# Optimization experiments

Hardware: AMD Instinct MI355X
Metric: run time of the kernel (lower is better)

Reference implementation:

```python
import jax, jax.numpy as jnp
import numpy as np

B, T, C, H = 16, 512, 1080, 20  # batch, seq, embd, heads; head_dim = C // H = 54

def setup_inputs() -> dict:
    key = jax.random.key(0)
    k1, k2, k3, k4, k5 = jax.random.split(key, 5)
    s = 0.02
    return {
        "x": jax.random.normal(k1, (B, T, C), dtype=jnp.float32),
        "W_attn": jax.random.normal(k2, (C, 3 * C), dtype=jnp.float32) * s,
        "b_attn": jax.random.normal(k3, (3 * C,), dtype=jnp.float32) * s,
        "W_proj": jax.random.normal(k4, (C, C), dtype=jnp.float32) * s,
        "b_proj": jax.random.normal(k5, (C,), dtype=jnp.float32) * s,
    }

def reference(x, W_attn, b_attn, W_proj, b_proj):
    Bb, Tt, Cc = x.shape
    hd = Cc // H
    qkv = jnp.einsum('btc,cd->btd', x, W_attn) + b_attn  # [B,T,3C]
    q, k, v = jnp.split(qkv, 3, axis=2)
    # [B,T,C] -> [B,H,T,hd]
    q = q.reshape(Bb, Tt, H, hd).transpose(0, 2, 1, 3)
    k = k.reshape(Bb, Tt, H, hd).transpose(0, 2, 1, 3)
    v = v.reshape(Bb, Tt, H, hd).transpose(0, 2, 1, 3)
    att = jnp.einsum('bhqd,bhkd->bhqk', q, k) * (1.0 / jnp.sqrt(jnp.float32(hd)))
    causal = jnp.tril(jnp.ones((Tt, Tt), dtype=bool))
    att = jnp.where(causal, att, -jnp.inf)
    att = jax.nn.softmax(att, axis=-1)
    y = jnp.einsum('bhqk,bhkd->bhqd', att, v)  # [B,H,T,hd]
    y = y.transpose(0, 2, 1, 3).reshape(Bb, Tt, Cc)
    return jnp.einsum('btc,cd->btd', y, W_proj) + b_proj
```

## Files before the change

kernel.cpp:

```cpp
#include <hip/hip_runtime.h>
#include <hip/hip_bf16.h>

#define B_   16
#define T_   512
#define C_   1080
#define H_   20
#define HD_  54
#define DP_  64
#define M_   (B_ * T_)
#define KP_  1088
#define NT_  17
#define NQKV_ 3840
#define NPRJ_ 1152
#define NBT_ (B_ * H_ * T_)

typedef short bf16x8 __attribute__((ext_vector_type(8)));
typedef float f32x4  __attribute__((ext_vector_type(4)));
typedef unsigned short u16x8 __attribute__((ext_vector_type(8)));

__device__ __forceinline__ void gload_lds16(const void* g, void* l) {
    __builtin_amdgcn_global_load_lds(
        (const __attribute__((address_space(1))) void*)g,
        (__attribute__((address_space(3))) void*)l,
        16, 0, 0);
}

__device__ __forceinline__ unsigned short f2b(float x) {
    return __builtin_bit_cast(unsigned short, __float2bfloat16(x));
}

__global__ __launch_bounds__(256) void cvt_pad(
    const float* __restrict__ src, __hip_bfloat16* __restrict__ dst)
{
    int idx = blockIdx.x * 256 + threadIdx.x;
    if (idx >= M_ * (KP_ / 4)) return;
    int m = idx / (KP_ / 4), c = idx - m * (KP_ / 4);
    ushort4 o;
    if (c < C_ / 4) {
        float4 v = *reinterpret_cast<const float4*>(src + (size_t)m * C_ + c * 4);
        o.x = f2b(v.x); o.y = f2b(v.y); o.z = f2b(v.z); o.w = f2b(v.w);
    } else {
        o.x = o.y = o.z = o.w = 0;
    }
    *reinterpret_cast<ushort4*>(reinterpret_cast<unsigned short*>(dst) + (size_t)m * KP_ + c * 4) = o;
}

__global__ __launch_bounds__(256) void transpose_wqkv(
    const float* __restrict__ W, __hip_bfloat16* __restrict__ Wt)
{
    __shared__ float tile[32][33];
    int n0 = blockIdx.x * 32, k0 = blockIdx.y * 32;
    int tx = threadIdx.x, ty = threadIdx.y;
    int np = n0 + tx;
    int which = np / 1280;
    int rem = np - which * 1280;
    int h = rem >> 6, d = rem & 63;
    int sn = which * C_ + h * HD_ + d;
    bool valid = d < HD_;
    #pragma unroll
    for (int i = 0; i < 32; i += 8) {
        int k = k0 + ty + i;
        tile[ty + i][tx] = (valid && k < C_) ? W[(size_t)k * (3 * C_) + sn] : 0.f;
    }
    __syncthreads();
    #pragma unroll
    for (int i = 0; i < 32; i += 8) {
        int n = n0 + ty + i, k = k0 + tx;
        Wt[(size_t)n * KP_ + k] = __float2bfloat16(tile[tx][ty + i]);
    }
}

__global__ __launch_bounds__(256) void transpose_w(
    const float* __restrict__ W, __hip_bfloat16* __restrict__ Wt,
    int K, int N, int Kp)
{
    __shared__ float tile[32][33];
    int n0 = blockIdx.x * 32, k0 = blockIdx.y * 32;
    int tx = threadIdx.x, ty = threadIdx.y;
    #pragma unroll
    for (int i = 0; i < 32; i += 8) {
        int k = k0 + ty + i, n = n0 + tx;
        tile[ty + i][tx] = (k < K && n < N) ? W[(size_t)k * N + n] : 0.f;
    }
    __syncthreads();
    #pragma unroll
    for (int i = 0; i < 32; i += 8) {
        int n = n0 + ty + i, k = k0 + tx;
        Wt[(size_t)n * Kp + k] = __float2bfloat16(tile[tx][ty + i]);
    }
}

__global__ __launch_bounds__(256) void build_bias(
    const float* __restrict__ b_attn, float* __restrict__ bp)
{
    int i = blockIdx.x * 256 + threadIdx.x;
    if (i < NQKV_) {
        int which = i / 1280, rem = i - which * 1280;
        int h = rem >> 6, d = rem & 63;
        float v = (d < HD_) ? b_attn[which * C_ + h * HD_ + d] : 0.f;
        if (which == 2 && d == 63) v = 1.0f;
        bp[i] = v;
    }
}

__global__ __launch_bounds__(512, 2) void gemm256(
    const unsigned short* __restrict__ A,
    const unsigned short* __restrict__ Bt,
    const float* __restrict__ bias,
    unsigned short* __restrict__ outQ,
    unsigned short* __restrict__ outK,
    unsigned short* __restrict__ outV)
{
    __shared__ __align__(16) char smem[131072];

    const int tid  = threadIdx.x;
    const int lane = tid & 63;
    const int wv   = tid >> 6;
    const int wr   = wv >> 2;
    const int wc   = wv & 3;
    const int lq   = lane & 15;
    const int lg   = lane >> 4;

    const int id  = blockIdx.y * 15 + blockIdx.x;
    const int xcd = id & 7;
    const int j   = id >> 3;
    const int m0  = (xcd * 4 + (j & 3)) * 256;
    const int n0  = (j >> 2) * 256;

    unsigned gA[2], gB[2];
    const int ld0 = tid * 16, ld1 = tid * 16 + 8192;
    #pragma unroll
    for (int i = 0; i < 2; ++i) {
        int ci = tid + i * 512;
        int r  = ci >> 3;
        int kc = (ci & 7) ^ (r & 7);
        gA[i] = (unsigned)(m0 + r) * KP_ + kc * 8;
        gB[i] = (unsigned)(n0 + r) * KP_ + kc * 8;
    }
    const unsigned HALFSTEP = 128u * KP_;

    auto stage = [&](int buf, int hIdx, unsigned k0) {
        char* sb = smem + buf * 65536 +
                   (hIdx < 2 ? hIdx * 16384 : 32768 + (hIdx - 2) * 16384);
        const unsigned short* sp = (hIdx < 2) ? A : Bt;
        unsigned extra = (hIdx & 1) ? HALFSTEP : 0u;
        gload_lds16(sp + ((hIdx < 2) ? gA[0] : gB[0]) + extra + k0, sb + ld0);
        gload_lds16(sp + ((hIdx < 2) ? gA[1] : gB[1]) + extra + k0, sb + ld1);
    };

    const int s0 = (lg ^ (lq & 7)) * 16;
    const int s1 = ((4 + lg) ^ (lq & 7)) * 16;
    const int aBase = wr * 16384 + lq * 128;
    const int bBase = 32768 + (wc >> 1) * 16384 + (wc & 1) * 8192 + lq * 128;

    f32x4 acc[8][4] = {};

    stage(0, 0, 0); stage(0, 1, 0); stage(0, 2, 0); stage(0, 3, 0);
    asm volatile("s_waitcnt vmcnt(0)" ::: "memory");
    __builtin_amdgcn_s_barrier();

    for (int t = 0; t < NT_; ++t) {
        const int cur = t & 1, nxt = cur ^ 1;
        const bool pf = (t + 1 < NT_);
        const unsigned k0n = (unsigned)(t + 1) * 64;
        const char* Ab = smem + cur * 65536 + aBase;
        const char* Bb = smem + cur * 65536 + bBase;

        bf16x8 bfr[4][2];
        #pragma unroll
        for (int p = 0; p < 4; ++p) {
            if (p == 0 && pf) { stage(nxt, 0, k0n); stage(nxt, 1, k0n); }
            if (p == 1 && pf) { stage(nxt, 2, k0n); stage(nxt, 3, k0n); }

            bf16x8 af[2][2];
            #pragma unroll
            for (int i = 0; i < 2; ++i) {
                int mi = p * 2 + i;
                af[0][i] = *reinterpret_cast<const bf16x8*>(Ab + mi * 2048 + s0);
                af[1][i] = *reinterpret_cast<const bf16x8*>(Ab + mi * 2048 + s1);
            }
            if (p == 0) {
                #pragma unroll
                for (int ni = 0; ni < 4; ++ni) {
                    bfr[ni][0] = *reinterpret_cast<const bf16x8*>(Bb + ni * 2048 + s0);
                    bfr[ni][1] = *reinterpret_cast<const bf16x8*>(Bb + ni * 2048 + s1);
                }
            }

            __builtin_amdgcn_s_barrier();
            asm volatile("s_waitcnt lgkmcnt(0)" ::: "memory");
            __builtin_amdgcn_sched_barrier(0);
            __builtin_amdgcn_s_setprio(1);
            #pragma unroll
            for (int kk = 0; kk < 2; ++kk)
                #pragma unroll
                for (int i = 0; i < 2; ++i)
                    #pragma unroll
                    for (int ni = 0; ni < 4; ++ni)
                        acc[p * 2 + i][ni] = __builtin_amdgcn_mfma_f32_16x16x32_bf16(
                            af[kk][i], bfr[ni][kk], acc[p * 2 + i][ni], 0, 0, 0);
            __builtin_amdgcn_s_setprio(0);
            if (p == 3) asm volatile("s_waitcnt vmcnt(0)" ::: "memory");
            __builtin_amdgcn_s_barrier();
        }
    }

    const int which = n0 / 1280;
    if (which < 2) {
        unsigned short* dst = which ? outK : outQ;
        #pragma unroll
        for (int mi = 0; mi < 8; ++mi) {
            int mg = m0 + wr * 128 + mi * 16 + lg * 4;
            int b = mg >> 9, t0 = mg & (T_ - 1);
            #pragma unroll
            for (int ni = 0; ni < 4; ++ni) {
                int nl = wc * 64 + ni * 16 + lq;
                int ng = n0 + nl - which * 1280;
                int h = ng >> 6, d = ng & 63;
                float bs = bias[n0 + nl];
                size_t basei = ((size_t)(b * H_ + h) * T_ + t0) * DP_ + d;
                #pragma unroll
                for (int j2 = 0; j2 < 4; ++j2)
                    dst[basei + (size_t)j2 * DP_] = f2b(acc[mi][ni][j2] + bs);
            }
        }
    } else {
        unsigned short* lt = (unsigned short*)smem;
        #pragma unroll
        for (int hm = 0; hm < 2; ++hm) {
            if (hm == 1) __syncthreads();
            if (wr == hm) {
                #pragma unroll
                for (int mi = 0; mi < 8; ++mi) {
                    int ml = mi * 16 + lg * 4;
                    int mc = ml >> 3, mo = ml & 7;
                    #pragma unroll
                    for (int ni = 0; ni < 4; ++ni) {
                        int nl = wc * 64 + ni * 16 + lq;
                        float bs = bias[n0 + nl];
                        ushort4 pk;
                        pk.x = f2b(acc[mi][ni][0] + bs);
                        pk.y = f2b(acc[mi][ni][1] + bs);
                        pk.z = f2b(acc[mi][ni][2] + bs);
                        pk.w = f2b(acc[mi][ni][3] + bs);
                        int slot = mc ^ ((nl >> 3) & 15);
                        *reinterpret_cast<ushort4*>(lt + nl * 136 + slot * 8 + mo) = pk;
                    }
                }
            }
            __syncthreads();
            #pragma unroll
            for (int it = 0; it < 8; ++it) {
                int idx = it * 512 + tid;
                int c2 = idx >> 4, j2 = idx & 15;
                int slot = j2 ^ ((c2 >> 3) & 15);
                u16x8 v = *reinterpret_cast<const u16x8*>(lt + c2 * 136 + slot * 8);
                int ng = n0 + c2 - 2560;
                int h = ng >> 6, d = ng & 63;
                int mg = m0 + hm * 128 + j2 * 8;
                int b = mg >> 9, t = mg & (T_ - 1);
                *reinterpret_cast<u16x8*>(outV + ((size_t)(b * H_ + h) * DP_ + d) * T_ + t) = v;
            }
        }
    }
}

__global__ __launch_bounds__(256) void gemm_mfma_p(
    const unsigned short* __restrict__ A,
    const unsigned short* __restrict__ Bt,
    const float* __restrict__ bias,
    float* __restrict__ outP)
{
    __shared__ __align__(16) char smem[65536];

    const int tid  = threadIdx.x;
    const int lane = tid & 63;
    const int wv   = tid >> 6;
    const int wm   = (wv >> 1) * 64;
    const int wn   = (wv & 1) * 64;
    const int lr   = lane & 15;
    const int lk   = lane >> 4;

    const int gx  = gridDim.x;
    const int gy  = gridDim.y;
    const int id  = blockIdx.y * gx + blockIdx.x;
    const int xcd = id & 7;
    const int j   = id >> 3;
    const int mpc = gy >> 3;
    const int m0  = (xcd * mpc + j % mpc) * 128;
    const int n0  = (j / mpc) * 128;

    unsigned aOff[4], bOff[4];
    int ciB[4];
    #pragma unroll
    for (int it = 0; it < 4; ++it) {
        int ci = it * 256 + tid;
        int r = ci >> 3, p = ci & 7;
        int kc = p ^ (r & 7);
        aOff[it] = (unsigned)(m0 + r) * KP_ + kc * 8;
        bOff[it] = (unsigned)(n0 + r) * KP_ + kc * 8;
        ciB[it] = ci * 16;
    }
    int aRd[2][4], bRd[2][4];
    #pragma unroll
    for (int kk = 0; kk < 2; ++kk) {
        #pragma unroll
        for (int mi = 0; mi < 4; ++mi) {
            int row = wm + mi * 16 + lr;
            aRd[kk][mi] = row * 128 + ((kk * 4 + lk) ^ (row & 7)) * 16;
            int rowb = wn + mi * 16 + lr;
            bRd[kk][mi] = 16384 + rowb * 128 + ((kk * 4 + lk) ^ (rowb & 7)) * 16;
        }
    }

    f32x4 acc[4][4] = {};

    auto stage = [&](int buf, int kt) {
        const unsigned k0 = kt * 64;
        char* sb = smem + buf * 32768;
        #pragma unroll
        for (int it = 0; it < 4; ++it)
            gload_lds16(A + aOff[it] + k0, sb + ciB[it]);
        #pragma unroll
        for (int it = 0; it < 4; ++it)
            gload_lds16(Bt + bOff[it] + k0, sb + 16384 + ciB[it]);
    };

    stage(0, 0);
    for (int kt = 0; kt < NT_; ++kt) {
        const int c = kt & 1;
        if (kt + 1 < NT_) {
            stage(1 - c, kt + 1);
            asm volatile("s_waitcnt vmcnt(8)" ::: "memory");
        } else {
            asm volatile("s_waitcnt vmcnt(0)" ::: "memory");
        }
        __builtin_amdgcn_s_barrier();
        asm volatile("" ::: "memory");

        const char* base = smem + c * 32768;
        #pragma unroll
        for (int kk = 0; kk < 2; ++kk) {
            bf16x8 af[4], bfr[4];
            #pragma unroll
            for (int mi = 0; mi < 4; ++mi)
                af[mi] = *reinterpret_cast<const bf16x8*>(base + aRd[kk][mi]);
            #pragma unroll
            for (int ni = 0; ni < 4; ++ni)
                bfr[ni] = *reinterpret_cast<const bf16x8*>(base + bRd[kk][ni]);
            #pragma unroll
            for (int mi = 0; mi < 4; ++mi)
                #pragma unroll
                for (int ni = 0; ni < 4; ++ni)
                    acc[mi][ni] = __builtin_amdgcn_mfma_f32_16x16x32_bf16(
                        af[mi], bfr[ni], acc[mi][ni], 0, 0, 0);
        }
        asm volatile("" ::: "memory");
        __builtin_amdgcn_s_barrier();
    }

    #pragma unroll
    for (int mi = 0; mi < 4; ++mi) {
        int mrow = m0 + wm + mi * 16 + lk * 4;
        #pragma unroll
        for (int ni = 0; ni < 4; ++ni) {
            int n = n0 + wn + ni * 16 + lr;
            if (n < C_) {
                float bs = bias[n];
                #pragma unroll
                for (int j2 = 0; j2 < 4; ++j2)
                    outP[(size_t)(mrow + j2) * C_ + n] = acc[mi][ni][j2] + bs;
            }
        }
    }
}

__global__ __launch_bounds__(256) void attn_mfma(
    const unsigned short* __restrict__ Q, const unsigned short* __restrict__ K,
    const unsigned short* __restrict__ Vt, __hip_bfloat16* __restrict__ Y)
{
    __shared__ __align__(16) char kvs[16384];
    __shared__ __align__(16) unsigned short ps[4][16][72];

    const int tid  = threadIdx.x;
    const int lane = tid & 63;
    const int wv   = tid >> 6;
    const int lq   = lane & 15;
    const int lg   = lane >> 4;
    const int bh   = blockIdx.y;
    const int qt   = blockIdx.x;
    const int qbase = qt * 64;
    const float cs = 0.13608276348795434f * 1.44269504f;

    bf16x8 qf[2];
    {
        const unsigned short* qp = Q + ((size_t)bh * T_ + qbase + wv * 16 + lq) * DP_;
        qf[0] = *reinterpret_cast<const bf16x8*>(qp + lg * 8);
        qf[1] = *reinterpret_cast<const bf16x8*>(qp + 32 + lg * 8);
    }

    unsigned kOff[2], vOff[2];
    int ciB[2];
    #pragma unroll
    for (int it = 0; it < 2; ++it) {
        int ci = it * 256 + tid;
        int r = ci >> 3, p = ci & 7;
        int pc = p ^ (r & 7);
        kOff[it] = (unsigned)(r * DP_ + pc * 8);
        vOff[it] = (unsigned)(r * T_ + pc * 8);
        ciB[it] = ci * 16;
    }
    const unsigned short* Kb = K  + (size_t)bh * T_ * DP_;
    const unsigned short* Vb = Vt + (size_t)bh * DP_ * T_;

    f32x4 o[4] = {};
    unsigned short* pbase = &ps[wv][0][0];
    const int nt = qt + 1;

    for (int kt = 0; kt < nt; ++kt) {
        const int kbase = kt * 64;
        #pragma unroll
        for (int it = 0; it < 2; ++it)
            gload_lds16(Kb + kOff[it] + (unsigned)kbase * DP_, kvs + ciB[it]);
        #pragma unroll
        for (int it = 0; it < 2; ++it)
            gload_lds16(Vb + vOff[it] + (unsigned)kbase, kvs + 8192 + ciB[it]);
        __syncthreads();

        f32x4 s[4] = {};
        #pragma unroll
        for (int dc = 0; dc < 2; ++dc) {
            #pragma unroll
            for (int ni = 0; ni < 4; ++ni) {
                int row = ni * 16 + lq;
                int ch  = (dc * 4 + lg) ^ (row & 7);
                bf16x8 kf = *reinterpret_cast<const bf16x8*>(kvs + row * 128 + ch * 16);
                s[ni] = __builtin_amdgcn_mfma_f32_16x16x32_bf16(qf[dc], kf, s[ni], 0, 0, 0);
            }
        }

        if (kt == qt) {
            #pragma unroll
            for (int ni = 0; ni < 4; ++ni) {
                int kg = kbase + ni * 16 + lq;
                #pragma unroll
                for (int j = 0; j < 4; ++j) {
                    int qg = qbase + wv * 16 + lg * 4 + j;
                    s[ni][j] = (kg > qg) ? -3.0e38f : s[ni][j];
                }
            }
        }
        #pragma unroll
        for (int ni = 0; ni < 4; ++ni) {
            #pragma unroll
            for (int j = 0; j < 4; ++j) {
                float p = exp2f(s[ni][j] * cs);
                int qr = lg * 4 + j;
                int cidx = (ni * 2 + (lq >> 3)) ^ (qr & 7);
                pbase[qr * 72 + cidx * 8 + (lq & 7)] = f2b(p);
            }
        }

        asm volatile("s_waitcnt lgkmcnt(0)" ::: "memory");
        __builtin_amdgcn_sched_barrier(0);

        #pragma unroll
        for (int dc = 0; dc < 2; ++dc) {
            int cc = (dc * 4 + lg) ^ (lq & 7);
            bf16x8 pf = *reinterpret_cast<const bf16x8*>(pbase + lq * 72 + cc * 8);
            #pragma unroll
            for (int ni = 0; ni < 4; ++ni) {
                int row = ni * 16 + lq;
                int ch  = (dc * 4 + lg) ^ (row & 7);
                bf16x8 vf = *reinterpret_cast<const bf16x8*>(kvs + 8192 + row * 128 + ch * 16);
                o[ni] = __builtin_amdgcn_mfma_f32_16x16x32_bf16(pf, vf, o[ni], 0, 0, 0);
            }
        }
        __syncthreads();
    }

    const int b = bh / H_, h = bh - b * H_;
    #pragma unroll
    for (int j = 0; j < 4; ++j) {
        float l = __shfl(o[3][j], (lane & 48) | 15, 64);
        float inv = 1.f / l;
        int t = qbase + wv * 16 + lg * 4 + j;
        #pragma unroll
        for (int ni = 0; ni < 4; ++ni) {
            int d = ni * 16 + lq;
            if (d < HD_)
                Y[((size_t)b * T_ + t) * KP_ + h * HD_ + d] =
                    __float2bfloat16(o[ni][j] * inv);
        }
    }
}

extern "C" void kernel_launch(void* const* d_in, const int* in_sizes, int n_in,
                              void* d_out, int out_size, void* d_ws, size_t ws_size,
                              hipStream_t stream)
{
    const float* x      = (const float*)d_in[0];
    const float* W_attn = (const float*)d_in[1];
    const float* b_attn = (const float*)d_in[2];
    const float* W_proj = (const float*)d_in[3];
    const float* b_proj = (const float*)d_in[4];
    float* out = (float*)d_out;

    __hip_bfloat16* xb = (__hip_bfloat16*)d_ws;
    unsigned short* qb = (unsigned short*)(xb + (size_t)M_ * KP_);
    unsigned short* kb = qb + (size_t)NBT_ * DP_;
    unsigned short* vtb = kb + (size_t)NBT_ * DP_;
    __hip_bfloat16* wta = (__hip_bfloat16*)(vtb + (size_t)NBT_ * DP_);
    __hip_bfloat16* wtp = wta + (size_t)NQKV_ * KP_;
    float* bp = (float*)(wtp + (size_t)NPRJ_ * KP_);
    __hip_bfloat16* yb = xb;

    cvt_pad<<<(M_ * (KP_ / 4) + 255) / 256, 256, 0, stream>>>(x, xb);
    transpose_wqkv<<<dim3(NQKV_ / 32, KP_ / 32), dim3(32, 8), 0, stream>>>(W_attn, wta);
    transpose_w<<<dim3(NPRJ_ / 32, KP_ / 32), dim3(32, 8), 0, stream>>>(
        W_proj, wtp, C_, C_, KP_);
    build_bias<<<(NQKV_ + 255) / 256, 256, 0, stream>>>(b_attn, bp);

    gemm256<<<dim3(NQKV_ / 256, M_ / 256), 512, 0, stream>>>(
        (const unsigned short*)xb, (const unsigned short*)wta, bp,
        qb, kb, vtb);

    attn_mfma<<<dim3(T_ / 64, B_ * H_), 256, 0, stream>>>(qb, kb, vtb, yb);

    gemm_mfma_p<<<dim3(NPRJ_ / 128, M_ / 128), 256, 0, stream>>>(
        (const unsigned short*)yb, (const unsigned short*)wtp, b_proj, out);
}
```

Before: 185.2 us.

## Restructure QKV GEMM main loop with single barrier and register double-buffered A fragments

The QKV GEMM k-loop now issues all global-to-LDS prefetches for the next tile at the start of each iteration. It waits with a partial vmcnt so the current tile is resident, then uses a single barrier instead of two barriers per sub-phase. A fragments are double-buffered in registers (afA/afB), so LDS reads for the next row block overlap with MFMAs on the current one. The aim is to cut barrier stalls and exposed LDS latency. In exchange it uses more VGPRs and relies on the compiler to place lgkmcnt waits correctly.

Measured after the change: 186.1 us. Within noise of the previous version (+0.5%).

```diff
diff --git a/kernel.cpp b/kernel.cpp
--- a/kernel.cpp
+++ b/kernel.cpp
@@ -156,53 +156,61 @@
     f32x4 acc[8][4] = {};
 
     stage(0, 0, 0); stage(0, 1, 0); stage(0, 2, 0); stage(0, 3, 0);
-    asm volatile("s_waitcnt vmcnt(0)" ::: "memory");
-    __builtin_amdgcn_s_barrier();
 
     for (int t = 0; t < NT_; ++t) {
-        const int cur = t & 1, nxt = cur ^ 1;
-        const bool pf = (t + 1 < NT_);
-        const unsigned k0n = (unsigned)(t + 1) * 64;
+        const int cur = t & 1;
+        if (t + 1 < NT_) {
+            const int nb = cur ^ 1;
+            const unsigned k0n = (unsigned)(t + 1) * 64;
+            stage(nb, 0, k0n); stage(nb, 1, k0n); stage(nb, 2, k0n); stage(nb, 3, k0n);
+            asm volatile("s_waitcnt vmcnt(8)" ::: "memory");
+        } else {
+            asm volatile("s_waitcnt vmcnt(0)" ::: "memory");
+        }
+        __builtin_amdgcn_s_barrier();
+
         const char* Ab = smem + cur * 65536 + aBase;
         const char* Bb = smem + cur * 65536 + bBase;
 
         bf16x8 bfr[4][2];
         #pragma unroll
-        for (int p = 0; p < 4; ++p) {
-            if (p == 0 && pf) { stage(nxt, 0, k0n); stage(nxt, 1, k0n); }
-            if (p == 1 && pf) { stage(nxt, 2, k0n); stage(nxt, 3, k0n); }
-
-            bf16x8 af[2][2];
-            #pragma unroll
-            for (int i = 0; i < 2; ++i) {
-                int mi = p * 2 + i;
-                af[0][i] = *reinterpret_cast<const bf16x8*>(Ab + mi * 2048 + s0);
-                af[1][i] = *reinterpret_cast<const bf16x8*>(Ab + mi * 2048 + s1);
-            }
-            if (p == 0) {
-                #pragma unroll
-                for (int ni = 0; ni < 4; ++ni) {
-                    bfr[ni][0] = *reinterpret_cast<const bf16x8*>(Bb + ni * 2048 + s0);
-                    bfr[ni][1] = *reinterpret_cast<const bf16x8*>(Bb + ni * 2048 + s1);
+        for (int ni = 0; ni < 4; ++ni) {
+            bfr[ni][0] = *reinterpret_cast<const bf16x8*>(Bb + ni * 2048 + s0);
+            bfr[ni][1] = *reinterpret_cast<const bf16x8*>(Bb + ni * 2048 + s1);
+        }
+        bf16x8 afA[2][2], afB[2][2];
+        #pragma unroll
+        for (int i = 0; i < 2; ++i) {
+            afA[0][i] = *reinterpret_cast<const bf16x8*>(Ab + i * 2048 + s0);
+            afA[1][i] = *reinterpret_cast<const bf16x8*>(Ab + i * 2048 + s1);
+        }
+        __builtin_amdgcn_s_setprio(1);
+        #pragma unroll
+        for (int q = 0; q < 4; ++q) {
+            if (q < 3) {
+                #pragma unroll
+                for (int i = 0; i < 2; ++i) {
+                    if (q & 1) {
+                        afA[0][i] = *reinterpret_cast<const bf16x8*>(Ab + ((q + 1) * 2 + i) * 2048 + s0);
+                        afA[1][i] = *reinterpret_cast<const bf16x8*>(Ab + ((q + 1) * 2 + i) * 2048 + s1);
+                    } else {
+                        afB[0][i] = *reinterpret_cast<const bf16x8*>(Ab + ((q + 1) * 2 + i) * 2048 + s0);
+                        afB[1][i] = *reinterpret_cast<const bf16x8*>(Ab + ((q + 1) * 2 + i) * 2048 + s1);
+                    }
                 }
             }
-
-            __builtin_amdgcn_s_barrier();
-            asm volatile("s_waitcnt lgkmcnt(0)" ::: "memory");
-            __builtin_amdgcn_sched_barrier(0);
-            __builtin_amdgcn_s_setprio(1);
             #pragma unroll
             for (int kk = 0; kk < 2; ++kk)
                 #pragma unroll
                 for (int i = 0; i < 2; ++i)
                     #pragma unroll
                     for (int ni = 0; ni < 4; ++ni)
-                        acc[p * 2 + i][ni] = __builtin_amdgcn_mfma_f32_16x16x32_bf16(
-                            af[kk][i], bfr[ni][kk], acc[p * 2 + i][ni], 0, 0, 0);
-            __builtin_amdgcn_s_setprio(0);
-            if (p == 3) asm volatile("s_waitcnt vmcnt(0)" ::: "memory");
-            __builtin_amdgcn_s_barrier();
-        }
+                        acc[q * 2 + i][ni] = __builtin_amdgcn_mfma_f32_16x16x32_bf16(
+                            (q & 1) ? afB[kk][i] : afA[kk][i], bfr[ni][kk],
+                            acc[q * 2 + i][ni], 0, 0, 0);
+        }
+        __builtin_amdgcn_s_setprio(0);
+        __builtin_amdgcn_s_barrier();
     }
 
     const int which = n0 / 1280;
```
